# Kernel tuning notes

Hardware: AMD Instinct MI355X
Metric: run time of the kernel (lower is better)

Reference implementation:

```python
import jax, jax.numpy as jnp
import numpy as np

N = 50000      # nodes
E = 800000     # edges
D = 128        # node_dim
H = 4          # heads
C = 64         # hidden_dim per head
B = 64         # graphs in batch
OUT = 10       # output_dim
SLOPE = 0.2    # GATConv leaky_relu negative slope (PyG default)


def gat_conv(x, src, dst, W, a_src, a_dst, bias, concat):
    """One PyG-style GATConv layer. src/dst already include self-loops."""
    n = x.shape[0]
    h = (x @ W).reshape(n, H, C)                       # [N,H,C]
    al_s = jnp.sum(h * a_src, axis=-1)                  # [N,H]
    al_d = jnp.sum(h * a_dst, axis=-1)                  # [N,H]
    e = jax.nn.leaky_relu(al_s[src] + al_d[dst], SLOPE)  # [E+N,H]
    m = jax.ops.segment_max(e, dst, num_segments=n)      # per-target-node max
    e = jnp.exp(e - m[dst])
    den = jax.ops.segment_sum(e, dst, num_segments=n)
    alpha = e / (den[dst] + 1e-16)                       # [E+N,H]
    msg = h[src] * alpha[:, :, None]                     # [E+N,H,C]
    out = jax.ops.segment_sum(msg, dst, num_segments=n)  # [N,H,C]
    out = out.reshape(n, H * C) if concat else out.mean(axis=1)
    return out + bias


def gat_forward(x, edge_index, batch, W0, b0, as0, ad0, W1, b1, as1, ad1,
                W2, b2, as2, ad2, pW1, pb1, pW2, pb2):
    n = x.shape[0]
    loop = jnp.arange(n, dtype=edge_index.dtype)
    src = jnp.concatenate([edge_index[0], loop])
    dst = jnp.concatenate([edge_index[1], loop])

    h = gat_conv(x, src, dst, W0, as0, ad0, b0, concat=True)
    h = jax.nn.elu(h)                                    # dropout = identity (eval)
    h = gat_conv(h, src, dst, W1, as1, ad1, b1, concat=True)
    h = jax.nn.elu(h)
    h = gat_conv(h, src, dst, W2, as2, ad2, b2, concat=False)  # [N,C]

    # global_mean_pool
    sums = jax.ops.segment_sum(h, batch, num_segments=B)        # [B,C]
    cnt = jax.ops.segment_sum(jnp.ones((n,), h.dtype), batch, num_segments=B)
    pooled = sums / jnp.maximum(cnt, 1.0)[:, None]

    # predictor MLP
    z = jax.nn.relu(pooled @ pW1 + pb1)
    return z @ pW2 + pb2                                        # [B,OUT]


def setup_inputs() -> dict:
    key = jax.random.key(0)
    ks = jax.random.split(key, 24)
    gl = lambda k, shp, fan: (jax.random.normal(k, shp, jnp.float32) / np.float32(np.sqrt(fan)))
    x = jax.random.normal(ks[0], (N, D), jnp.float32)
    edge_index = jax.random.randint(ks[1], (2, E), 0, N, dtype=jnp.int32)
    batch = jnp.sort(jax.random.randint(ks[2], (N,), 0, B, dtype=jnp.int32))
    return dict(
        x=x, edge_index=edge_index, batch=batch,
        W0=gl(ks[3], (D, H * C), D), b0=jnp.zeros((H * C,), jnp.float32),
        as0=gl(ks[4], (H, C), C), ad0=gl(ks[5], (H, C), C),
        W1=gl(ks[6], (H * C, H * C), H * C), b1=jnp.zeros((H * C,), jnp.float32),
        as1=gl(ks[7], (H, C), C), ad1=gl(ks[8], (H, C), C),
        W2=gl(ks[9], (H * C, H * C), H * C), b2=jnp.zeros((C,), jnp.float32),
        as2=gl(ks[10], (H, C), C), ad2=gl(ks[11], (H, C), C),
        pW1=gl(ks[12], (C, C // 2), C), pb1=jnp.zeros((C // 2,), jnp.float32),
        pW2=gl(ks[13], (C // 2, OUT), C // 2), pb2=jnp.zeros((OUT,), jnp.float32),
    )


def reference(x, edge_index, batch, W0, b0, as0, ad0, W1, b1, as1, ad1,
              W2, b2, as2, ad2, pW1, pb1, pW2, pb2):
    return gat_forward(x, edge_index, batch, W0, b0, as0, ad0, W1, b1, as1, ad1,
                       W2, b2, as2, ad2, pW1, pb1, pW2, pb2)
```

## Files before the change

kernel.cpp:

```cpp
#include <hip/hip_runtime.h>
#include <hip/hip_fp16.h>
#include <cstdint>

#define N_NODES 50000
#define E_EDGES 800000
#define HC 256
#define B_GR 64
#define OUT_DIM 10
#define SLOPE 0.2f
#define NBLK_SCAN ((N_NODES + 255) / 256)

using f16x8 = __attribute__((ext_vector_type(8))) _Float16;
using f32x4 = __attribute__((ext_vector_type(4))) float;

#define GLOAD_LDS16(gsrc, ldst) \
    __builtin_amdgcn_global_load_lds((const __attribute__((address_space(1))) void*)(gsrc), \
        (__attribute__((address_space(3))) void*)(ldst), 16, 0, 0)

__device__ inline void wsplit_one(const float* W, _Float16* wh, _Float16* wl,
                                  int K, int i) {
    int k = i >> 8, n = i & 255;
    float v = W[i];
    _Float16 h = (_Float16)v;
    _Float16 l = (_Float16)(v - (float)h);
    int oidx = ((((k >> 5) * 256 + n) * 4) + ((k >> 3) & 3)) * 8 + (k & 7);
    wh[oidx] = h;
    wl[oidx] = l;
}

__global__ void prep_split(const float* __restrict__ x,
        _Float16* __restrict__ xhi, _Float16* __restrict__ xlo,
        const float* __restrict__ W0, _Float16* __restrict__ w0h, _Float16* __restrict__ w0l,
        const float* __restrict__ W1, _Float16* __restrict__ w1h, _Float16* __restrict__ w1l,
        const float* __restrict__ W2, _Float16* __restrict__ w2h, _Float16* __restrict__ w2l) {
    const int NX = N_NODES * 128;
    int i = blockIdx.x * 256 + threadIdx.x;
    if (i < NX) {
        float v = x[i];
        _Float16 h = (_Float16)v;
        xhi[i] = h;
        xlo[i] = (_Float16)(v - (float)h);
        return;
    }
    int j = i - NX;
    if (j < 128 * 256) { wsplit_one(W0, w0h, w0l, 128, j); return; }
    j -= 128 * 256;
    if (j < 256 * 256) { wsplit_one(W1, w1h, w1l, 256, j); return; }
    j -= 256 * 256;
    if (j < 256 * 256) { wsplit_one(W2, w2h, w2l, 256, j); return; }
}

template<int K, int TERMS>
__global__ __launch_bounds__(256) void gemm16(const _Float16* __restrict__ Ahi,
        const _Float16* __restrict__ Alo,
        const _Float16* __restrict__ wt_hi, const _Float16* __restrict__ wt_lo,
        __half* __restrict__ h_half,
        const float* __restrict__ a_src, const float* __restrict__ a_dst,
        float* __restrict__ al_s, float* __restrict__ al_d, int M) {
    __shared__ _Float16 abuf[2][2][64][64];
    int tid = threadIdx.x;
    int w = tid >> 6;
    int l = tid & 63;
    int rr = l & 15;
    int kg = l >> 4;
    int row0 = blockIdx.x * 64;
    int srow = tid >> 3;
    int sgs  = tid & 7;

    f32x4 acc[4][4] = {};
    const int NT = K / 64;

    auto stage = [&](int buf, int t) {
        int k0 = t * 64;
#pragma unroll
        for (int i = 0; i < 2; ++i) {
            int row = i * 32 + srow;
            int g = sgs ^ (row & 7);
            int gr = min(row0 + row, M - 1);
            char* dst = (char*)abuf + buf * 16384 + i * 4096 + w * 1024;
            GLOAD_LDS16(&Ahi[(size_t)gr * K + k0 + g * 8], dst);
            if constexpr (TERMS == 3)
                GLOAD_LDS16(&Alo[(size_t)gr * K + k0 + g * 8], dst + 8192);
        }
    };

    stage(0, 0);
    __syncthreads();
    int cur = 0;
    for (int t = 0; t < NT; ++t) {
        if (t + 1 < NT) stage(cur ^ 1, t + 1);
        const _Float16* base_hi = &abuf[cur][0][0][0];
        const _Float16* base_lo = &abuf[cur][1][0][0];
#pragma unroll
        for (int c = 0; c < 2; ++c) {
            f16x8 ah[4], alo_[4];
#pragma unroll
            for (int fm = 0; fm < 4; ++fm) {
                int row = fm * 16 + rr;
                int gsw = ((c * 4 + kg) ^ (row & 7));
                ah[fm] = *(const f16x8*)&base_hi[row * 64 + gsw * 8];
                if constexpr (TERMS == 3)
                    alo_[fm] = *(const f16x8*)&base_lo[row * 64 + gsw * 8];
            }
            int chunk = t * 2 + c;
#pragma unroll
            for (int fn = 0; fn < 4; ++fn) {
                int col = w * 64 + fn * 16 + rr;
                size_t boff = (((size_t)chunk * 256 + col) * 4 + kg) * 8;
                f16x8 bh = *(const f16x8*)&wt_hi[boff];
                f16x8 bl = *(const f16x8*)&wt_lo[boff];
#pragma unroll
                for (int fm = 0; fm < 4; ++fm) {
                    acc[fm][fn] = __builtin_amdgcn_mfma_f32_16x16x32_f16(ah[fm], bh, acc[fm][fn], 0, 0, 0);
                    acc[fm][fn] = __builtin_amdgcn_mfma_f32_16x16x32_f16(ah[fm], bl, acc[fm][fn], 0, 0, 0);
                    if constexpr (TERMS == 3)
                        acc[fm][fn] = __builtin_amdgcn_mfma_f32_16x16x32_f16(alo_[fm], bh, acc[fm][fn], 0, 0, 0);
                }
            }
        }
        __syncthreads();
        cur ^= 1;
    }

    int head = w;
    float asv[4], adv[4];
#pragma unroll
    for (int fn = 0; fn < 4; ++fn) {
        asv[fn] = a_src[head * 64 + fn * 16 + rr];
        adv[fn] = a_dst[head * 64 + fn * 16 + rr];
    }
#pragma unroll
    for (int fm = 0; fm < 4; ++fm) {
#pragma unroll
        for (int r = 0; r < 4; ++r) {
            int row = fm * 16 + kg * 4 + r;
            int gr = row0 + row;
            float ps = acc[fm][0][r] * asv[0] + acc[fm][1][r] * asv[1]
                     + acc[fm][2][r] * asv[2] + acc[fm][3][r] * asv[3];
            float pd = acc[fm][0][r] * adv[0] + acc[fm][1][r] * adv[1]
                     + acc[fm][2][r] * adv[2] + acc[fm][3][r] * adv[3];
#pragma unroll
            for (int off = 1; off < 16; off <<= 1) {
                ps += __shfl_xor(ps, off, 64);
                pd += __shfl_xor(pd, off, 64);
            }
            if (gr < M) {
#pragma unroll
                for (int fn = 0; fn < 4; ++fn)
                    h_half[(size_t)gr * HC + w * 64 + fn * 16 + rr] = __float2half(acc[fm][fn][r]);
                if (rr == 0) {
                    al_s[gr * 4 + head] = ps;
                    al_d[gr * 4 + head] = pd;
                }
            }
        }
    }
}

__global__ void init_cnt(int* cnt) {
    int i = blockIdx.x * blockDim.x + threadIdx.x;
    if (i < N_NODES) cnt[i] = 1;
}
__global__ void hist_kernel(const int* __restrict__ dsts, int* cnt) {
    int i = blockIdx.x * blockDim.x + threadIdx.x;
    if (i < E_EDGES) atomicAdd(&cnt[dsts[i]], 1);
}
__global__ __launch_bounds__(256) void scan_bsum(const int* __restrict__ cnt,
                                                 int* __restrict__ bsum) {
    __shared__ int ws[4];
    int t = threadIdx.x;
    int i = blockIdx.x * 256 + t;
    int v = (i < N_NODES) ? cnt[i] : 0;
#pragma unroll
    for (int off = 1; off < 64; off <<= 1) v += __shfl_xor(v, off, 64);
    if ((t & 63) == 0) ws[t >> 6] = v;
    __syncthreads();
    if (t == 0) bsum[blockIdx.x] = ws[0] + ws[1] + ws[2] + ws[3];
}
__global__ __launch_bounds__(256) void scan_boff(const int* __restrict__ bsum,
                                                 int* __restrict__ boff) {
    __shared__ int s[256];
    int t = threadIdx.x;
    int v = (t < NBLK_SCAN) ? bsum[t] : 0;
    s[t] = v;
    __syncthreads();
    for (int off = 1; off < 256; off <<= 1) {
        int u = (t >= off) ? s[t - off] : 0;
        __syncthreads();
        s[t] += u;
        __syncthreads();
    }
    if (t < NBLK_SCAN) boff[t] = s[t] - v;
}
__global__ __launch_bounds__(256) void scan_final(const int* __restrict__ cnt,
        const int* __restrict__ boff, int* __restrict__ row_ptr,
        int* __restrict__ cursor) {
    __shared__ int s[256];
    int b = blockIdx.x, t = threadIdx.x;
    int i = b * 256 + t;
    int v = (i < N_NODES) ? cnt[i] : 0;
    s[t] = v;
    __syncthreads();
    for (int off = 1; off < 256; off <<= 1) {
        int u = (t >= off) ? s[t - off] : 0;
        __syncthreads();
        s[t] += u;
        __syncthreads();
    }
    int rp = boff[b] + s[t] - v;
    if (i < N_NODES) { row_ptr[i] = rp; cursor[i] = rp; }
    if (i == N_NODES - 1) row_ptr[N_NODES] = rp + v;
}
__global__ void scatter_kernel(const int* __restrict__ srcs, const int* __restrict__ dsts,
                               int* cursor, int* col) {
    int i = blockIdx.x * blockDim.x + threadIdx.x;
    if (i >= E_EDGES + N_NODES) return;
    int s, d;
    if (i < E_EDGES) { s = srcs[i]; d = dsts[i]; }
    else             { s = d = i - E_EDGES; }
    int pos = atomicAdd(&cursor[d], 1);
    col[pos] = s;
}

__global__ __launch_bounds__(256) void agg_kernel(const __half* __restrict__ hh,
        const float* __restrict__ al_s, const float* __restrict__ al_d,
        const int* __restrict__ row_ptr, const int* __restrict__ col,
        const float* __restrict__ bias, _Float16* __restrict__ out_h,
        float* __restrict__ out_f, int mode) {
    __shared__ int   lds_col[4][64];
    __shared__ float lds_alpha[4][64][4];
    int wid  = threadIdx.x >> 6;
    int lane = threadIdx.x & 63;
    int hf   = lane >> 5;
    int ln   = lane & 31;
    int nodeA = blockIdx.x * 8 + wid * 2;
    int nodeB = nodeA + 1;
    int sA = row_ptr[nodeA], eA = row_ptr[nodeA + 1];
    int sB = row_ptr[nodeB], eB = row_ptr[nodeB + 1];
    int degA = eA - sA, degB = eB - sB;

    if (degA <= 32 && degB <= 32) {
        int node  = hf ? nodeB : nodeA;
        int start = hf ? sB : sA;
        int deg   = hf ? degB : degA;
        int degmax = max(degA, degB);
        const float4 ald = *(const float4*)&al_d[node * 4];
        bool active = ln < deg;
        int s = active ? col[start + ln] : 0;
        float4 as = *(const float4*)&al_s[s * 4];
        float e0 = as.x + ald.x; e0 = e0 > 0.f ? e0 : SLOPE * e0;
        float e1 = as.y + ald.y; e1 = e1 > 0.f ? e1 : SLOPE * e1;
        float e2 = as.z + ald.z; e2 = e2 > 0.f ? e2 : SLOPE * e2;
        float e3 = as.w + ald.w; e3 = e3 > 0.f ? e3 : SLOPE * e3;
        float m0 = active ? e0 : -1e30f, m1 = active ? e1 : -1e30f;
        float m2 = active ? e2 : -1e30f, m3 = active ? e3 : -1e30f;
#pragma unroll
        for (int off = 1; off < 32; off <<= 1) {
            m0 = fmaxf(m0, __shfl_xor(m0, off, 64));
            m1 = fmaxf(m1, __shfl_xor(m1, off, 64));
            m2 = fmaxf(m2, __shfl_xor(m2, off, 64));
            m3 = fmaxf(m3, __shfl_xor(m3, off, 64));
        }
        float x0 = active ? expf(e0 - m0) : 0.f;
        float x1 = active ? expf(e1 - m1) : 0.f;
        float x2 = active ? expf(e2 - m2) : 0.f;
        float x3 = active ? expf(e3 - m3) : 0.f;
        float d0 = x0, d1 = x1, d2 = x2, d3 = x3;
#pragma unroll
        for (int off = 1; off < 32; off <<= 1) {
            d0 += __shfl_xor(d0, off, 64);
            d1 += __shfl_xor(d1, off, 64);
            d2 += __shfl_xor(d2, off, 64);
            d3 += __shfl_xor(d3, off, 64);
        }
        float4 a4;
        a4.x = x0 / (d0 + 1e-16f); a4.y = x1 / (d1 + 1e-16f);
        a4.z = x2 / (d2 + 1e-16f); a4.w = x3 / (d3 + 1e-16f);
        int e = hf * 32 + ln;
        lds_col[wid][e] = s;
        *(float4*)&lds_alpha[wid][e][0] = a4;
        int head = ln >> 3;
        int ch0 = ln * 8;
        float acc[8] = {0.f, 0.f, 0.f, 0.f, 0.f, 0.f, 0.f, 0.f};
        int ebase = hf * 32;
        for (int t0 = 0; t0 < degmax; t0 += 4) {
            float wv[4]; float4 raw[4];
#pragma unroll
            for (int k = 0; k < 4; ++k) {
                int t = t0 + k;
                int tt = min(t, deg - 1);
                int s2 = lds_col[wid][ebase + tt];
                wv[k] = (t < deg) ? lds_alpha[wid][ebase + tt][head] : 0.f;
                raw[k] = *(const float4*)&hh[(size_t)s2 * HC + ch0];
            }
#pragma unroll
            for (int k = 0; k < 4; ++k) {
                const __half2* hp = (const __half2*)&raw[k];
                float2 f0 = __half22float2(hp[0]);
                float2 f1 = __half22float2(hp[1]);
                float2 f2 = __half22float2(hp[2]);
                float2 f3 = __half22float2(hp[3]);
                acc[0] = fmaf(wv[k], f0.x, acc[0]); acc[1] = fmaf(wv[k], f0.y, acc[1]);
                acc[2] = fmaf(wv[k], f1.x, acc[2]); acc[3] = fmaf(wv[k], f1.y, acc[3]);
                acc[4] = fmaf(wv[k], f2.x, acc[4]); acc[5] = fmaf(wv[k], f2.y, acc[5]);
                acc[6] = fmaf(wv[k], f3.x, acc[6]); acc[7] = fmaf(wv[k], f3.y, acc[7]);
            }
        }
        if (mode == 0) {
            float b8[8];
            *(float4*)&b8[0] = *(const float4*)&bias[ch0];
            *(float4*)&b8[4] = *(const float4*)&bias[ch0 + 4];
            _Float16 v[8];
#pragma unroll
            for (int j = 0; j < 8; ++j) {
                float t = acc[j] + b8[j];
                v[j] = (_Float16)(t > 0.f ? t : expm1f(t));
            }
            *(float4*)&out_h[(size_t)node * HC + ch0] = *(float4*)v;
        } else {
#pragma unroll
            for (int j = 0; j < 8; ++j) {
                acc[j] += __shfl_xor(acc[j], 8, 64);
                acc[j] += __shfl_xor(acc[j], 16, 64);
            }
            if (ln < 8) {
                float v[8];
#pragma unroll
                for (int j = 0; j < 8; ++j)
                    v[j] = acc[j] * 0.25f + bias[ln * 8 + j];
                *(float4*)&out_f[(size_t)node * 64 + ln * 8]     = *(float4*)&v[0];
                *(float4*)&out_f[(size_t)node * 64 + ln * 8 + 4] = *(float4*)&v[4];
            }
        }
        return;
    }

    for (int nn = 0; nn < 2; ++nn) {
        int node = nodeA + nn;
        int start = row_ptr[node], end = row_ptr[node + 1];
        int deg = end - start;
        const float4 ald = *(const float4*)&al_d[node * 4];
        int head = lane >> 4;
        float ald_h = head == 0 ? ald.x : head == 1 ? ald.y : head == 2 ? ald.z : ald.w;
        float ax = 0.f, ay = 0.f, az = 0.f, aw = 0.f;

        if (deg <= 64) {
            int j = start + lane;
            bool active = j < end;
            int s = active ? col[j] : 0;
            float4 as = *(const float4*)&al_s[s * 4];
            float e0 = as.x + ald.x; e0 = e0 > 0.f ? e0 : SLOPE * e0;
            float e1 = as.y + ald.y; e1 = e1 > 0.f ? e1 : SLOPE * e1;
            float e2 = as.z + ald.z; e2 = e2 > 0.f ? e2 : SLOPE * e2;
            float e3 = as.w + ald.w; e3 = e3 > 0.f ? e3 : SLOPE * e3;
            float m0 = active ? e0 : -1e30f, m1 = active ? e1 : -1e30f;
            float m2 = active ? e2 : -1e30f, m3 = active ? e3 : -1e30f;
#pragma unroll
            for (int off = 1; off < 64; off <<= 1) {
                m0 = fmaxf(m0, __shfl_xor(m0, off, 64));
                m1 = fmaxf(m1, __shfl_xor(m1, off, 64));
                m2 = fmaxf(m2, __shfl_xor(m2, off, 64));
                m3 = fmaxf(m3, __shfl_xor(m3, off, 64));
            }
            float x0 = active ? expf(e0 - m0) : 0.f;
            float x1 = active ? expf(e1 - m1) : 0.f;
            float x2 = active ? expf(e2 - m2) : 0.f;
            float x3 = active ? expf(e3 - m3) : 0.f;
            float d0 = x0, d1 = x1, d2 = x2, d3 = x3;
#pragma unroll
            for (int off = 1; off < 64; off <<= 1) {
                d0 += __shfl_xor(d0, off, 64);
                d1 += __shfl_xor(d1, off, 64);
                d2 += __shfl_xor(d2, off, 64);
                d3 += __shfl_xor(d3, off, 64);
            }
            float4 a4;
            a4.x = x0 / (d0 + 1e-16f); a4.y = x1 / (d1 + 1e-16f);
            a4.z = x2 / (d2 + 1e-16f); a4.w = x3 / (d3 + 1e-16f);
            lds_col[wid][lane] = s;
            *(float4*)&lds_alpha[wid][lane][0] = a4;
            for (int t0 = 0; t0 < deg; t0 += 8) {
                int nr = deg - t0;
                float wv[8]; float2 raw[8];
#pragma unroll
                for (int k = 0; k < 8; ++k) {
                    if (k < nr) {
                        int s2 = lds_col[wid][t0 + k];
                        wv[k] = lds_alpha[wid][t0 + k][head];
                        raw[k] = *(const float2*)&hh[(size_t)s2 * HC + lane * 4];
                    } else {
                        wv[k] = 0.f;
                        raw[k] = make_float2(0.f, 0.f);
                    }
                }
#pragma unroll
                for (int k = 0; k < 8; ++k) {
                    float2 f0 = __half22float2(*(__half2*)&raw[k].x);
                    float2 f1 = __half22float2(*(__half2*)&raw[k].y);
                    ax = fmaf(wv[k], f0.x, ax); ay = fmaf(wv[k], f0.y, ay);
                    az = fmaf(wv[k], f1.x, az); aw = fmaf(wv[k], f1.y, aw);
                }
            }
        } else {
            float m0 = -1e30f, m1 = -1e30f, m2 = -1e30f, m3 = -1e30f;
            for (int j = start + lane; j < end; j += 64) {
                int s = col[j];
                float4 as = *(const float4*)&al_s[s * 4];
                float e0 = as.x + ald.x; e0 = e0 > 0.f ? e0 : SLOPE * e0;
                float e1 = as.y + ald.y; e1 = e1 > 0.f ? e1 : SLOPE * e1;
                float e2 = as.z + ald.z; e2 = e2 > 0.f ? e2 : SLOPE * e2;
                float e3 = as.w + ald.w; e3 = e3 > 0.f ? e3 : SLOPE * e3;
                m0 = fmaxf(m0, e0); m1 = fmaxf(m1, e1);
                m2 = fmaxf(m2, e2); m3 = fmaxf(m3, e3);
            }
#pragma unroll
            for (int off = 1; off < 64; off <<= 1) {
                m0 = fmaxf(m0, __shfl_xor(m0, off, 64));
                m1 = fmaxf(m1, __shfl_xor(m1, off, 64));
                m2 = fmaxf(m2, __shfl_xor(m2, off, 64));
                m3 = fmaxf(m3, __shfl_xor(m3, off, 64));
            }
            float d0 = 0.f, d1 = 0.f, d2 = 0.f, d3 = 0.f;
            for (int j = start + lane; j < end; j += 64) {
                int s = col[j];
                float4 as = *(const float4*)&al_s[s * 4];
                float e0 = as.x + ald.x; e0 = e0 > 0.f ? e0 : SLOPE * e0;
                float e1 = as.y + ald.y; e1 = e1 > 0.f ? e1 : SLOPE * e1;
                float e2 = as.z + ald.z; e2 = e2 > 0.f ? e2 : SLOPE * e2;
                float e3 = as.w + ald.w; e3 = e3 > 0.f ? e3 : SLOPE * e3;
                d0 += expf(e0 - m0); d1 += expf(e1 - m1);
                d2 += expf(e2 - m2); d3 += expf(e3 - m3);
            }
#pragma unroll
            for (int off = 1; off < 64; off <<= 1) {
                d0 += __shfl_xor(d0, off, 64);
                d1 += __shfl_xor(d1, off, 64);
                d2 += __shfl_xor(d2, off, 64);
                d3 += __shfl_xor(d3, off, 64);
            }
            float inv0 = 1.f / (d0 + 1e-16f), inv1 = 1.f / (d1 + 1e-16f);
            float inv2 = 1.f / (d2 + 1e-16f), inv3 = 1.f / (d3 + 1e-16f);
            float m_h   = head == 0 ? m0   : head == 1 ? m1   : head == 2 ? m2   : m3;
            float inv_h = head == 0 ? inv0 : head == 1 ? inv1 : head == 2 ? inv2 : inv3;
            for (int jb = start; jb < end; jb += 64) {
                int j = jb + lane;
                int cs = (j < end) ? col[j] : 0;
                int cnt2 = min(64, end - jb);
                for (int t = 0; t < cnt2; ++t) {
                    int s = __shfl(cs, t, 64);
                    float als2 = al_s[s * 4 + head];
                    float e = als2 + ald_h; e = e > 0.f ? e : SLOPE * e;
                    float wv = expf(e - m_h) * inv_h;
                    float2 raw = *(const float2*)&hh[(size_t)s * HC + lane * 4];
                    float2 f0 = __half22float2(*(__half2*)&raw.x);
                    float2 f1 = __half22float2(*(__half2*)&raw.y);
                    ax = fmaf(wv, f0.x, ax); ay = fmaf(wv, f0.y, ay);
                    az = fmaf(wv, f1.x, az); aw = fmaf(wv, f1.y, aw);
                }
            }
        }

        if (mode == 0) {
            float4 b4 = *(const float4*)&bias[lane * 4];
            float vx = ax + b4.x; vx = vx > 0.f ? vx : expm1f(vx);
            float vy = ay + b4.y; vy = vy > 0.f ? vy : expm1f(vy);
            float vz = az + b4.z; vz = vz > 0.f ? vz : expm1f(vz);
            float vw = aw + b4.w; vw = vw > 0.f ? vw : expm1f(vw);
            _Float16 v[4] = {(_Float16)vx, (_Float16)vy, (_Float16)vz, (_Float16)vw};
            *(float2*)&out_h[(size_t)node * HC + lane * 4] = *(float2*)v;
        } else {
#pragma unroll
            for (int off = 16; off < 64; off <<= 1) {
                ax += __shfl_xor(ax, off, 64);
                ay += __shfl_xor(ay, off, 64);
                az += __shfl_xor(az, off, 64);
                aw += __shfl_xor(aw, off, 64);
            }
            if (lane < 16) {
                float4 b4 = *(const float4*)&bias[lane * 4];
                float4 v = make_float4(ax * 0.25f + b4.x, ay * 0.25f + b4.y,
                                       az * 0.25f + b4.z, aw * 0.25f + b4.w);
                *(float4*)&out_f[(size_t)node * 64 + lane * 4] = v;
            }
        }
    }
}

__global__ __launch_bounds__(1024) void pool_kernel(const float* __restrict__ act,
        const int* __restrict__ batch, float* __restrict__ pooled) {
    __shared__ float part[16][64];
    int b = blockIdx.x;
    int warp = threadIdx.x >> 6;
    int lane = threadIdx.x & 63;
    int lo = 0, hi = N_NODES;
    while (lo < hi) { int mid = (lo + hi) >> 1; if (batch[mid] < b) lo = mid + 1; else hi = mid; }
    int s = lo;
    lo = 0; hi = N_NODES;
    while (lo < hi) { int mid = (lo + hi) >> 1; if (batch[mid] < b + 1) lo = mid + 1; else hi = mid; }
    int e = lo;
    float sum = 0.f;
    for (int n = s + warp; n < e; n += 16)
        sum += act[(size_t)n * 64 + lane];
    part[warp][lane] = sum;
    __syncthreads();
    if (threadIdx.x < 64) {
        float t = 0.f;
#pragma unroll
        for (int r = 0; r < 16; ++r) t += part[r][lane];
        pooled[b * 64 + lane] = t;
    }
}

__global__ __launch_bounds__(64) void mlp_kernel(const float* __restrict__ pooled,
        const int* __restrict__ batch,
        const float* __restrict__ pW1, const float* __restrict__ pb1,
        const float* __restrict__ pW2, const float* __restrict__ pb2,
        float* __restrict__ outp) {
    __shared__ float p[64];
    __shared__ float z[32];
    int b = blockIdx.x, t = threadIdx.x;
    int lo = 0, hi = N_NODES;
    while (lo < hi) { int mid = (lo + hi) >> 1; if (batch[mid] < b) lo = mid + 1; else hi = mid; }
    int s = lo;
    lo = 0; hi = N_NODES;
    while (lo < hi) { int mid = (lo + hi) >> 1; if (batch[mid] < b + 1) lo = mid + 1; else hi = mid; }
    int e = lo;
    float inv = 1.f / (float)max(e - s, 1);
    p[t] = pooled[b * 64 + t] * inv;
    __syncthreads();
    if (t < 32) {
        float s2 = pb1[t];
        for (int c = 0; c < 64; ++c) s2 += p[c] * pW1[c * 32 + t];
        z[t] = s2 > 0.f ? s2 : 0.f;
    }
    __syncthreads();
    if (t < OUT_DIM) {
        float s2 = pb2[t];
        for (int k = 0; k < 32; ++k) s2 += z[k] * pW2[k * 10 + t];
        outp[b * 10 + t] = s2;
    }
}

extern "C" void kernel_launch(void* const* d_in, const int* in_sizes, int n_in,
                              void* d_out, int out_size, void* d_ws, size_t ws_size,
                              hipStream_t stream) {
    const float* x    = (const float*)d_in[0];
    const int*   ei   = (const int*)d_in[1];
    const int*   batch= (const int*)d_in[2];
    const float* W0   = (const float*)d_in[3];
    const float* b0   = (const float*)d_in[4];
    const float* as0  = (const float*)d_in[5];
    const float* ad0  = (const float*)d_in[6];
    const float* W1   = (const float*)d_in[7];
    const float* b1   = (const float*)d_in[8];
    const float* as1  = (const float*)d_in[9];
    const float* ad1  = (const float*)d_in[10];
    const float* W2   = (const float*)d_in[11];
    const float* b2   = (const float*)d_in[12];
    const float* as2  = (const float*)d_in[13];
    const float* ad2  = (const float*)d_in[14];
    const float* pW1  = (const float*)d_in[15];
    const float* pb1  = (const float*)d_in[16];
    const float* pW2  = (const float*)d_in[17];
    const float* pb2  = (const float*)d_in[18];
    float* out = (float*)d_out;

    char* ws = (char*)d_ws;
    size_t off = 0;
    auto alloc = [&](size_t bytes) -> void* {
        void* p = ws + off;
        off += (bytes + 255) & ~(size_t)255;
        return p;
    };
    __half*    h_half = (__half*)alloc((size_t)N_NODES * HC * 2);
    _Float16*  act_h  = (_Float16*)alloc((size_t)N_NODES * HC * 2);
    float*     act_f  = (float*)alloc((size_t)N_NODES * 64 * 4);
    _Float16*  xhi    = (_Float16*)alloc((size_t)N_NODES * 128 * 2);
    _Float16*  xlo    = (_Float16*)alloc((size_t)N_NODES * 128 * 2);
    float* als    = (float*)alloc((size_t)N_NODES * 4 * 4);
    float* ald    = (float*)alloc((size_t)N_NODES * 4 * 4);
    int*   cnt    = (int*)alloc((size_t)N_NODES * 4);
    int*   row_ptr= (int*)alloc((size_t)(N_NODES + 1) * 4);
    int*   cursor = (int*)alloc((size_t)N_NODES * 4);
    int*   col    = (int*)alloc((size_t)(E_EDGES + N_NODES) * 4);
    float* pooled = (float*)alloc((size_t)B_GR * 64 * 4);
    int*   bsum   = (int*)alloc((size_t)NBLK_SCAN * 4);
    int*   boff   = (int*)alloc((size_t)NBLK_SCAN * 4);
    _Float16* w0h = (_Float16*)alloc((size_t)128 * 256 * 2);
    _Float16* w0l = (_Float16*)alloc((size_t)128 * 256 * 2);
    _Float16* w1h = (_Float16*)alloc((size_t)256 * 256 * 2);
    _Float16* w1l = (_Float16*)alloc((size_t)256 * 256 * 2);
    _Float16* w2h = (_Float16*)alloc((size_t)256 * 256 * 2);
    _Float16* w2l = (_Float16*)alloc((size_t)256 * 256 * 2);

    const int* srcs = ei;
    const int* dsts = ei + E_EDGES;

    const int PREP_N = N_NODES * 128 + 128 * 256 + 256 * 256 + 256 * 256;
    prep_split<<<(PREP_N + 255) / 256, 256, 0, stream>>>(
        x, xhi, xlo, W0, w0h, w0l, W1, w1h, w1l, W2, w2h, w2l);

    init_cnt<<<(N_NODES + 255) / 256, 256, 0, stream>>>(cnt);
    hist_kernel<<<(E_EDGES + 255) / 256, 256, 0, stream>>>(dsts, cnt);
    scan_bsum<<<NBLK_SCAN, 256, 0, stream>>>(cnt, bsum);
    scan_boff<<<1, 256, 0, stream>>>(bsum, boff);
    scan_final<<<NBLK_SCAN, 256, 0, stream>>>(cnt, boff, row_ptr, cursor);
    scatter_kernel<<<(E_EDGES + N_NODES + 255) / 256, 256, 0, stream>>>(srcs, dsts, cursor, col);

    int gblk = (N_NODES + 63) / 64;
    int nblk = (N_NODES + 7) / 8;

    gemm16<128, 3><<<gblk, 256, 0, stream>>>(xhi, xlo, w0h, w0l, h_half, as0, ad0, als, ald, N_NODES);
    agg_kernel<<<nblk, 256, 0, stream>>>(h_half, als, ald, row_ptr, col, b0, act_h, act_f, 0);
    gemm16<256, 2><<<gblk, 256, 0, stream>>>(act_h, nullptr, w1h, w1l, h_half, as1, ad1, als, ald, N_NODES);
    agg_kernel<<<nblk, 256, 0, stream>>>(h_half, als, ald, row_ptr, col, b1, act_h, act_f, 0);
    gemm16<256, 2><<<gblk, 256, 0, stream>>>(act_h, nullptr, w2h, w2l, h_half, as2, ad2, als, ald, N_NODES);
    agg_kernel<<<nblk, 256, 0, stream>>>(h_half, als, ald, row_ptr, col, b2, act_h, act_f, 1);

    pool_kernel<<<B_GR, 1024, 0, stream>>>(act_f, batch, pooled);
    mlp_kernel<<<B_GR, 64, 0, stream>>>(pooled, batch, pW1, pb1, pW2, pb2, out);
}
```

Before: 423.1 us.

## Fuse GAT aggregation with next layer GEMM and merge pool/MLP kernels

Layers 1 and 2 now aggregate 64 destination nodes per block straight into a swizzled LDS activation tile, apply bias and ELU, and run the next layer's MFMA GEMM and attention projections from that tile. This removes the global write and re-read of the fp16 activation buffer and two kernel launches. Ping-pong h/al buffers avoid read-write hazards. The cnt init is folded into prep_split and pool and MLP are merged into one kernel. The trade-off is heavy LDS use (32KB+) and a long serial aggregation phase per block before the GEMM, with fewer blocks than before, which may reduce occupancy and latency hiding in the gather.

```diff
diff --git a/kernel.cpp b/kernel.cpp
--- a/kernel.cpp
+++ b/kernel.cpp
@@ -32,7 +32,8 @@
         _Float16* __restrict__ xhi, _Float16* __restrict__ xlo,
         const float* __restrict__ W0, _Float16* __restrict__ w0h, _Float16* __restrict__ w0l,
         const float* __restrict__ W1, _Float16* __restrict__ w1h, _Float16* __restrict__ w1l,
-        const float* __restrict__ W2, _Float16* __restrict__ w2h, _Float16* __restrict__ w2l) {
+        const float* __restrict__ W2, _Float16* __restrict__ w2h, _Float16* __restrict__ w2l,
+        int* __restrict__ cnt) {
     const int NX = N_NODES * 128;
     int i = blockIdx.x * 256 + threadIdx.x;
     if (i < NX) {
@@ -48,6 +49,8 @@
     if (j < 256 * 256) { wsplit_one(W1, w1h, w1l, 256, j); return; }
     j -= 256 * 256;
     if (j < 256 * 256) { wsplit_one(W2, w2h, w2l, 256, j); return; }
+    j -= 256 * 256;
+    if (j < N_NODES) cnt[j] = 1;
 }
 
 template<int K, int TERMS>
@@ -157,10 +160,326 @@
     }
 }
 
-__global__ void init_cnt(int* cnt) {
-    int i = blockIdx.x * blockDim.x + threadIdx.x;
-    if (i < N_NODES) cnt[i] = 1;
-}
+__global__ __launch_bounds__(256) void fused_agg_gemm(
+        const __half* __restrict__ hh,
+        const float* __restrict__ al_s, const float* __restrict__ al_d,
+        const int* __restrict__ row_ptr, const int* __restrict__ col,
+        const float* __restrict__ bias,
+        const _Float16* __restrict__ wt_hi, const _Float16* __restrict__ wt_lo,
+        __half* __restrict__ h_out,
+        const float* __restrict__ a_srcn, const float* __restrict__ a_dstn,
+        float* __restrict__ al_s_out, float* __restrict__ al_d_out, int M) {
+    __shared__ _Float16 a_act[64][256];
+    __shared__ int   lds_col[4][64];
+    __shared__ float lds_alpha[4][64][4];
+    int tid = threadIdx.x;
+    int wid = tid >> 6;
+    int lane = tid & 63;
+    int hf = lane >> 5;
+    int ln = lane & 31;
+    int row0 = blockIdx.x * 64;
+
+    for (int it = 0; it < 8; ++it) {
+        int nodeA = row0 + it * 8 + wid * 2;
+        int nodeB = nodeA + 1;
+        int rA = it * 8 + wid * 2, rB = rA + 1;
+        bool vA = nodeA < M, vB = nodeB < M;
+        int sA = 0, eA = 0, sB = 0, eB = 0;
+        if (vA) { sA = row_ptr[nodeA]; eA = row_ptr[nodeA + 1]; }
+        if (vB) { sB = row_ptr[nodeB]; eB = row_ptr[nodeB + 1]; }
+        int degA = eA - sA, degB = eB - sB;
+
+        if (degA <= 32 && degB <= 32) {
+            int node  = hf ? nodeB : nodeA;
+            int r     = hf ? rB : rA;
+            int start = hf ? sB : sA;
+            int deg   = hf ? degB : degA;
+            bool valid = hf ? vB : vA;
+            int degmax = max(degA, degB);
+            float4 ald = valid ? *(const float4*)&al_d[node * 4]
+                               : make_float4(0.f, 0.f, 0.f, 0.f);
+            bool active = ln < deg;
+            int s = active ? col[start + ln] : 0;
+            float4 as = *(const float4*)&al_s[s * 4];
+            float e0 = as.x + ald.x; e0 = e0 > 0.f ? e0 : SLOPE * e0;
+            float e1 = as.y + ald.y; e1 = e1 > 0.f ? e1 : SLOPE * e1;
+            float e2 = as.z + ald.z; e2 = e2 > 0.f ? e2 : SLOPE * e2;
+            float e3 = as.w + ald.w; e3 = e3 > 0.f ? e3 : SLOPE * e3;
+            float m0 = active ? e0 : -1e30f, m1 = active ? e1 : -1e30f;
+            float m2 = active ? e2 : -1e30f, m3 = active ? e3 : -1e30f;
+#pragma unroll
+            for (int off = 1; off < 32; off <<= 1) {
+                m0 = fmaxf(m0, __shfl_xor(m0, off, 64));
+                m1 = fmaxf(m1, __shfl_xor(m1, off, 64));
+                m2 = fmaxf(m2, __shfl_xor(m2, off, 64));
+                m3 = fmaxf(m3, __shfl_xor(m3, off, 64));
+            }
+            float x0 = active ? expf(e0 - m0) : 0.f;
+            float x1 = active ? expf(e1 - m1) : 0.f;
+            float x2 = active ? expf(e2 - m2) : 0.f;
+            float x3 = active ? expf(e3 - m3) : 0.f;
+            float d0 = x0, d1 = x1, d2 = x2, d3 = x3;
+#pragma unroll
+            for (int off = 1; off < 32; off <<= 1) {
+                d0 += __shfl_xor(d0, off, 64);
+                d1 += __shfl_xor(d1, off, 64);
+                d2 += __shfl_xor(d2, off, 64);
+                d3 += __shfl_xor(d3, off, 64);
+            }
+            float4 a4;
+            a4.x = x0 / (d0 + 1e-16f); a4.y = x1 / (d1 + 1e-16f);
+            a4.z = x2 / (d2 + 1e-16f); a4.w = x3 / (d3 + 1e-16f);
+            int e = hf * 32 + ln;
+            lds_col[wid][e] = s;
+            *(float4*)&lds_alpha[wid][e][0] = a4;
+            int head = ln >> 3;
+            int ch0 = ln * 8;
+            float acc[8] = {0.f, 0.f, 0.f, 0.f, 0.f, 0.f, 0.f, 0.f};
+            int ebase = hf * 32;
+            for (int t0 = 0; t0 < degmax; t0 += 4) {
+                float wv[4]; float4 raw[4];
+#pragma unroll
+                for (int k = 0; k < 4; ++k) {
+                    int t = t0 + k;
+                    int tt = max(min(t, deg - 1), 0);
+                    int s2 = lds_col[wid][ebase + tt];
+                    wv[k] = (t < deg) ? lds_alpha[wid][ebase + tt][head] : 0.f;
+                    raw[k] = *(const float4*)&hh[(size_t)s2 * HC + ch0];
+                }
+#pragma unroll
+                for (int k = 0; k < 4; ++k) {
+                    const __half2* hp = (const __half2*)&raw[k];
+                    float2 f0 = __half22float2(hp[0]);
+                    float2 f1 = __half22float2(hp[1]);
+                    float2 f2 = __half22float2(hp[2]);
+                    float2 f3 = __half22float2(hp[3]);
+                    acc[0] = fmaf(wv[k], f0.x, acc[0]); acc[1] = fmaf(wv[k], f0.y, acc[1]);
+                    acc[2] = fmaf(wv[k], f1.x, acc[2]); acc[3] = fmaf(wv[k], f1.y, acc[3]);
+                    acc[4] = fmaf(wv[k], f2.x, acc[4]); acc[5] = fmaf(wv[k], f2.y, acc[5]);
+                    acc[6] = fmaf(wv[k], f3.x, acc[6]); acc[7] = fmaf(wv[k], f3.y, acc[7]);
+                }
+            }
+            float b8[8];
+            *(float4*)&b8[0] = *(const float4*)&bias[ch0];
+            *(float4*)&b8[4] = *(const float4*)&bias[ch0 + 4];
+            f16x8 v;
+#pragma unroll
+            for (int j = 0; j < 8; ++j) {
+                float t = acc[j] + b8[j];
+                t = t > 0.f ? t : expm1f(t);
+                v[j] = valid ? (_Float16)t : (_Float16)0.f;
+            }
+            int gs = ln ^ (r & 7);
+            *(f16x8*)&a_act[r][gs * 8] = v;
+        } else {
+            for (int nn = 0; nn < 2; ++nn) {
+                int node = nodeA + nn;
+                int r = rA + nn;
+                bool valid = node < M;
+                int start = 0, end = 0;
+                if (valid) { start = row_ptr[node]; end = row_ptr[node + 1]; }
+                int deg = end - start;
+                float4 ald = valid ? *(const float4*)&al_d[node * 4]
+                                   : make_float4(0.f, 0.f, 0.f, 0.f);
+                int head = lane >> 4;
+                float ald_h = head == 0 ? ald.x : head == 1 ? ald.y : head == 2 ? ald.z : ald.w;
+                float ax = 0.f, ay = 0.f, az = 0.f, aw = 0.f;
+
+                if (deg <= 64) {
+                    int j = start + lane;
+                    bool active = lane < deg;
+                    int s = active ? col[j] : 0;
+                    float4 as = *(const float4*)&al_s[s * 4];
+                    float e0 = as.x + ald.x; e0 = e0 > 0.f ? e0 : SLOPE * e0;
+                    float e1 = as.y + ald.y; e1 = e1 > 0.f ? e1 : SLOPE * e1;
+                    float e2 = as.z + ald.z; e2 = e2 > 0.f ? e2 : SLOPE * e2;
+                    float e3 = as.w + ald.w; e3 = e3 > 0.f ? e3 : SLOPE * e3;
+                    float m0 = active ? e0 : -1e30f, m1 = active ? e1 : -1e30f;
+                    float m2 = active ? e2 : -1e30f, m3 = active ? e3 : -1e30f;
+#pragma unroll
+                    for (int off = 1; off < 64; off <<= 1) {
+                        m0 = fmaxf(m0, __shfl_xor(m0, off, 64));
+                        m1 = fmaxf(m1, __shfl_xor(m1, off, 64));
+                        m2 = fmaxf(m2, __shfl_xor(m2, off, 64));
+                        m3 = fmaxf(m3, __shfl_xor(m3, off, 64));
+                    }
+                    float x0 = active ? expf(e0 - m0) : 0.f;
+                    float x1 = active ? expf(e1 - m1) : 0.f;
+                    float x2 = active ? expf(e2 - m2) : 0.f;
+                    float x3 = active ? expf(e3 - m3) : 0.f;
+                    float d0 = x0, d1 = x1, d2 = x2, d3 = x3;
+#pragma unroll
+                    for (int off = 1; off < 64; off <<= 1) {
+                        d0 += __shfl_xor(d0, off, 64);
+                        d1 += __shfl_xor(d1, off, 64);
+                        d2 += __shfl_xor(d2, off, 64);
+                        d3 += __shfl_xor(d3, off, 64);
+                    }
+                    float4 a4;
+                    a4.x = x0 / (d0 + 1e-16f); a4.y = x1 / (d1 + 1e-16f);
+                    a4.z = x2 / (d2 + 1e-16f); a4.w = x3 / (d3 + 1e-16f);
+                    lds_col[wid][lane] = s;
+                    *(float4*)&lds_alpha[wid][lane][0] = a4;
+                    for (int t0 = 0; t0 < deg; t0 += 8) {
+                        int nr = deg - t0;
+                        float wv[8]; float2 raw[8];
+#pragma unroll
+                        for (int k = 0; k < 8; ++k) {
+                            if (k < nr) {
+                                int s2 = lds_col[wid][t0 + k];
+                                wv[k] = lds_alpha[wid][t0 + k][head];
+                                raw[k] = *(const float2*)&hh[(size_t)s2 * HC + lane * 4];
+                            } else {
+                                wv[k] = 0.f;
+                                raw[k] = make_float2(0.f, 0.f);
+                            }
+                        }
+#pragma unroll
+                        for (int k = 0; k < 8; ++k) {
+                            float2 f0 = __half22float2(*(__half2*)&raw[k].x);
+                            float2 f1 = __half22float2(*(__half2*)&raw[k].y);
+                            ax = fmaf(wv[k], f0.x, ax); ay = fmaf(wv[k], f0.y, ay);
+                            az = fmaf(wv[k], f1.x, az); aw = fmaf(wv[k], f1.y, aw);
+                        }
+                    }
+                } else {
+                    float m0 = -1e30f, m1 = -1e30f, m2 = -1e30f, m3 = -1e30f;
+                    for (int j = start + lane; j < end; j += 64) {
+                        int s = col[j];
+                        float4 as = *(const float4*)&al_s[s * 4];
+                        float e0 = as.x + ald.x; e0 = e0 > 0.f ? e0 : SLOPE * e0;
+                        float e1 = as.y + ald.y; e1 = e1 > 0.f ? e1 : SLOPE * e1;
+                        float e2 = as.z + ald.z; e2 = e2 > 0.f ? e2 : SLOPE * e2;
+                        float e3 = as.w + ald.w; e3 = e3 > 0.f ? e3 : SLOPE * e3;
+                        m0 = fmaxf(m0, e0); m1 = fmaxf(m1, e1);
+                        m2 = fmaxf(m2, e2); m3 = fmaxf(m3, e3);
+                    }
+#pragma unroll
+                    for (int off = 1; off < 64; off <<= 1) {
+                        m0 = fmaxf(m0, __shfl_xor(m0, off, 64));
+                        m1 = fmaxf(m1, __shfl_xor(m1, off, 64));
+                        m2 = fmaxf(m2, __shfl_xor(m2, off, 64));
+                        m3 = fmaxf(m3, __shfl_xor(m3, off, 64));
+                    }
+                    float d0 = 0.f, d1 = 0.f, d2 = 0.f, d3 = 0.f;
+                    for (int j = start + lane; j < end; j += 64) {
+                        int s = col[j];
+                        float4 as = *(const float4*)&al_s[s * 4];
+                        float e0 = as.x + ald.x; e0 = e0 > 0.f ? e0 : SLOPE * e0;
+                        float e1 = as.y + ald.y; e1 = e1 > 0.f ? e1 : SLOPE * e1;
+                        float e2 = as.z + ald.z; e2 = e2 > 0.f ? e2 : SLOPE * e2;
+                        float e3 = as.w + ald.w; e3 = e3 > 0.f ? e3 : SLOPE * e3;
+                        d0 += expf(e0 - m0); d1 += expf(e1 - m1);
+                        d2 += expf(e2 - m2); d3 += expf(e3 - m3);
+                    }
+#pragma unroll
+                    for (int off = 1; off < 64; off <<= 1) {
+                        d0 += __shfl_xor(d0, off, 64);
+                        d1 += __shfl_xor(d1, off, 64);
+                        d2 += __shfl_xor(d2, off, 64);
+                        d3 += __shfl_xor(d3, off, 64);
+                    }
+                    float inv0 = 1.f / (d0 + 1e-16f), inv1 = 1.f / (d1 + 1e-16f);
+                    float inv2 = 1.f / (d2 + 1e-16f), inv3 = 1.f / (d3 + 1e-16f);
+                    float m_h   = head == 0 ? m0   : head == 1 ? m1   : head == 2 ? m2   : m3;
+                    float inv_h = head == 0 ? inv0 : head == 1 ? inv1 : head == 2 ? inv2 : inv3;
+                    for (int jb = start; jb < end; jb += 64) {
+                        int j = jb + lane;
+                        int cs = (j < end) ? col[j] : 0;
+                        int cnt2 = min(64, end - jb);
+                        for (int t = 0; t < cnt2; ++t) {
+                            int s = __shfl(cs, t, 64);
+                            float als2 = al_s[s * 4 + head];
+                            float e = als2 + ald_h; e = e > 0.f ? e : SLOPE * e;
+                            float wv = expf(e - m_h) * inv_h;
+                            float2 raw = *(const float2*)&hh[(size_t)s * HC + lane * 4];
+                            float2 f0 = __half22float2(*(__half2*)&raw.x);
+                            float2 f1 = __half22float2(*(__half2*)&raw.y);
+                            ax = fmaf(wv, f0.x, ax); ay = fmaf(wv, f0.y, ay);
+                            az = fmaf(wv, f1.x, az); aw = fmaf(wv, f1.y, aw);
+                        }
+                    }
+                }
+                float4 b4 = *(const float4*)&bias[lane * 4];
+                float vx = ax + b4.x; vx = vx > 0.f ? vx : expm1f(vx);
+                float vy = ay + b4.y; vy = vy > 0.f ? vy : expm1f(vy);
+                float vz = az + b4.z; vz = vz > 0.f ? vz : expm1f(vz);
+                float vw = aw + b4.w; vw = vw > 0.f ? vw : expm1f(vw);
+                _Float16 v[4];
+                v[0] = valid ? (_Float16)vx : (_Float16)0.f;
+                v[1] = valid ? (_Float16)vy : (_Float16)0.f;
+                v[2] = valid ? (_Float16)vz : (_Float16)0.f;
+                v[3] = valid ? (_Float16)vw : (_Float16)0.f;
+                int grp = lane >> 1, half = lane & 1;
+                int gs = grp ^ (r & 7);
+                *(float2*)&a_act[r][gs * 8 + half * 4] = *(float2*)v;
+            }
+        }
+    }
+    __syncthreads();
+
+    int w = wid;
+    int rr = lane & 15;
+    int kg = lane >> 4;
+    f32x4 acc[4][4] = {};
+#pragma unroll
+    for (int ch = 0; ch < 8; ++ch) {
+        f16x8 ah[4];
+#pragma unroll
+        for (int fm = 0; fm < 4; ++fm) {
+            int row = fm * 16 + rr;
+            int gsw = ((ch * 4 + kg) ^ (row & 7));
+            ah[fm] = *(const f16x8*)&a_act[row][gsw * 8];
+        }
+#pragma unroll
+        for (int fn = 0; fn < 4; ++fn) {
+            int c2 = w * 64 + fn * 16 + rr;
+            size_t boff = (((size_t)ch * 256 + c2) * 4 + kg) * 8;
+            f16x8 bh = *(const f16x8*)&wt_hi[boff];
+            f16x8 bl = *(const f16x8*)&wt_lo[boff];
+#pragma unroll
+            for (int fm = 0; fm < 4; ++fm) {
+                acc[fm][fn] = __builtin_amdgcn_mfma_f32_16x16x32_f16(ah[fm], bh, acc[fm][fn], 0, 0, 0);
+                acc[fm][fn] = __builtin_amdgcn_mfma_f32_16x16x32_f16(ah[fm], bl, acc[fm][fn], 0, 0, 0);
+            }
+        }
+    }
+
+    int head = w;
+    float asv[4], adv[4];
+#pragma unroll
+    for (int fn = 0; fn < 4; ++fn) {
+        asv[fn] = a_srcn[head * 64 + fn * 16 + rr];
+        adv[fn] = a_dstn[head * 64 + fn * 16 + rr];
+    }
+#pragma unroll
+    for (int fm = 0; fm < 4; ++fm) {
+#pragma unroll
+        for (int r = 0; r < 4; ++r) {
+            int row = fm * 16 + kg * 4 + r;
+            int gr = row0 + row;
+            float ps = acc[fm][0][r] * asv[0] + acc[fm][1][r] * asv[1]
+                     + acc[fm][2][r] * asv[2] + acc[fm][3][r] * asv[3];
+            float pd = acc[fm][0][r] * adv[0] + acc[fm][1][r] * adv[1]
+                     + acc[fm][2][r] * adv[2] + acc[fm][3][r] * adv[3];
+#pragma unroll
+            for (int off = 1; off < 16; off <<= 1) {
+                ps += __shfl_xor(ps, off, 64);
+                pd += __shfl_xor(pd, off, 64);
+            }
+            if (gr < M) {
+#pragma unroll
+                for (int fn = 0; fn < 4; ++fn)
+                    h_out[(size_t)gr * HC + w * 64 + fn * 16 + rr] = __float2half(acc[fm][fn][r]);
+                if (rr == 0) {
+                    al_s_out[gr * 4 + head] = ps;
+                    al_d_out[gr * 4 + head] = pd;
+                }
+            }
+        }
+    }
+}
+
 __global__ void hist_kernel(const int* __restrict__ dsts, int* cnt) {
     int i = blockIdx.x * blockDim.x + threadIdx.x;
     if (i < E_EDGES) atomicAdd(&cnt[dsts[i]], 1);
@@ -222,11 +541,10 @@
     col[pos] = s;
 }
 
-__global__ __launch_bounds__(256) void agg_kernel(const __half* __restrict__ hh,
+__global__ __launch_bounds__(256) void agg_final(const __half* __restrict__ hh,
         const float* __restrict__ al_s, const float* __restrict__ al_d,
         const int* __restrict__ row_ptr, const int* __restrict__ col,
-        const float* __restrict__ bias, _Float16* __restrict__ out_h,
-        float* __restrict__ out_f, int mode) {
+        const float* __restrict__ bias, float* __restrict__ out_f) {
     __shared__ int   lds_col[4][64];
     __shared__ float lds_alpha[4][64][4];
     int wid  = threadIdx.x >> 6;
@@ -288,7 +606,7 @@
 #pragma unroll
             for (int k = 0; k < 4; ++k) {
                 int t = t0 + k;
-                int tt = min(t, deg - 1);
+                int tt = max(min(t, deg - 1), 0);
                 int s2 = lds_col[wid][ebase + tt];
                 wv[k] = (t < deg) ? lds_alpha[wid][ebase + tt][head] : 0.f;
                 raw[k] = *(const float4*)&hh[(size_t)s2 * HC + ch0];
@@ -306,31 +624,18 @@
                 acc[6] = fmaf(wv[k], f3.x, acc[6]); acc[7] = fmaf(wv[k], f3.y, acc[7]);
             }
         }
-        if (mode == 0) {
-            float b8[8];
-            *(float4*)&b8[0] = *(const float4*)&bias[ch0];
-            *(float4*)&b8[4] = *(const float4*)&bias[ch0 + 4];
-            _Float16 v[8];
-#pragma unroll
-            for (int j = 0; j < 8; ++j) {
-                float t = acc[j] + b8[j];
-                v[j] = (_Float16)(t > 0.f ? t : expm1f(t));
-            }
-            *(float4*)&out_h[(size_t)node * HC + ch0] = *(float4*)v;
-        } else {
-#pragma unroll
-            for (int j = 0; j < 8; ++j) {
-                acc[j] += __shfl_xor(acc[j], 8, 64);
-                acc[j] += __shfl_xor(acc[j], 16, 64);
-            }
-            if (ln < 8) {
-                float v[8];
-#pragma unroll
-                for (int j = 0; j < 8; ++j)
-                    v[j] = acc[j] * 0.25f + bias[ln * 8 + j];
-                *(float4*)&out_f[(size_t)node * 64 + ln * 8]     = *(float4*)&v[0];
-                *(float4*)&out_f[(size_t)node * 64 + ln * 8 + 4] = *(float4*)&v[4];
-            }
+#pragma unroll
+        for (int j = 0; j < 8; ++j) {
+            acc[j] += __shfl_xor(acc[j], 8, 64);
+            acc[j] += __shfl_xor(acc[j], 16, 64);
+        }
+        if (ln < 8) {
+            float v[8];
+#pragma unroll
+            for (int j = 0; j < 8; ++j)
+                v[j] = acc[j] * 0.25f + bias[ln * 8 + j];
+            *(float4*)&out_f[(size_t)node * 64 + ln * 8]     = *(float4*)&v[0];
+            *(float4*)&out_f[(size_t)node * 64 + ln * 8 + 4] = *(float4*)&v[4];
         }
         return;
     }
@@ -343,7 +648,6 @@
         int head = lane >> 4;
         float ald_h = head == 0 ? ald.x : head == 1 ? ald.y : head == 2 ? ald.z : ald.w;
         float ax = 0.f, ay = 0.f, az = 0.f, aw = 0.f;
-
         if (deg <= 64) {
             int j = start + lane;
             bool active = j < end;
@@ -459,36 +763,30 @@
                 }
             }
         }
-
-        if (mode == 0) {
+#pragma unroll
+        for (int off = 16; off < 64; off <<= 1) {
+            ax += __shfl_xor(ax, off, 64);
+            ay += __shfl_xor(ay, off, 64);
+            az += __shfl_xor(az, off, 64);
+            aw += __shfl_xor(aw, off, 64);
+        }
+        if (lane < 16) {
             float4 b4 = *(const float4*)&bias[lane * 4];
-            float vx = ax + b4.x; vx = vx > 0.f ? vx : expm1f(vx);
-            float vy = ay + b4.y; vy = vy > 0.f ? vy : expm1f(vy);
-            float vz = az + b4.z; vz = vz > 0.f ? vz : expm1f(vz);
-            float vw = aw + b4.w; vw = vw > 0.f ? vw : expm1f(vw);
-            _Float16 v[4] = {(_Float16)vx, (_Float16)vy, (_Float16)vz, (_Float16)vw};
-            *(float2*)&out_h[(size_t)node * HC + lane * 4] = *(float2*)v;
-        } else {
-#pragma unroll
-            for (int off = 16; off < 64; off <<= 1) {
-                ax += __shfl_xor(ax, off, 64);
-                ay += __shfl_xor(ay, off, 64);
-                az += __shfl_xor(az, off, 64);
-                aw += __shfl_xor(aw, off, 64);
-            }
-            if (lane < 16) {
-                float4 b4 = *(const float4*)&bias[lane * 4];
-                float4 v = make_float4(ax * 0.25f + b4.x, ay * 0.25f + b4.y,
-                                       az * 0.25f + b4.z, aw * 0.25f + b4.w);
-                *(float4*)&out_f[(size_t)node * 64 + lane * 4] = v;
-            }
-        }
-    }
-}
-
-__global__ __launch_bounds__(1024) void pool_kernel(const float* __restrict__ act,
-        const int* __restrict__ batch, float* __restrict__ pooled) {
+            float4 v = make_float4(ax * 0.25f + b4.x, ay * 0.25f + b4.y,
+                                   az * 0.25f + b4.z, aw * 0.25f + b4.w);
+            *(float4*)&out_f[(size_t)node * 64 + lane * 4] = v;
+        }
+    }
+}
+
+__global__ __launch_bounds__(1024) void poolmlp_kernel(const float* __restrict__ act,
+        const int* __restrict__ batch,
+        const float* __restrict__ pW1, const float* __restrict__ pb1,
+        const float* __restrict__ pW2, const float* __restrict__ pb2,
+        float* __restrict__ outp) {
     __shared__ float part[16][64];
+    __shared__ float p[64];
+    __shared__ float z[32];
     int b = blockIdx.x;
     int warp = threadIdx.x >> 6;
     int lane = threadIdx.x & 63;
@@ -503,30 +801,13 @@
         sum += act[(size_t)n * 64 + lane];
     part[warp][lane] = sum;
     __syncthreads();
-    if (threadIdx.x < 64) {
-        float t = 0.f;
-#pragma unroll
-        for (int r = 0; r < 16; ++r) t += part[r][lane];
-        pooled[b * 64 + lane] = t;
-    }
-}
-
-__global__ __launch_bounds__(64) void mlp_kernel(const float* __restrict__ pooled,
-        const int* __restrict__ batch,
-        const float* __restrict__ pW1, const float* __restrict__ pb1,
-        const float* __restrict__ pW2, const float* __restrict__ pb2,
-        float* __restrict__ outp) {
-    __shared__ float p[64];
-    __shared__ float z[32];
-    int b = blockIdx.x, t = threadIdx.x;
-    int lo = 0, hi = N_NODES;
-    while (lo < hi) { int mid = (lo + hi) >> 1; if (batch[mid] < b) lo = mid + 1; else hi = mid; }
-    int s = lo;
-    lo = 0; hi = N_NODES;
-    while (lo < hi) { int mid = (lo + hi) >> 1; if (batch[mid] < b + 1) lo = mid + 1; else hi = mid; }
-    int e = lo;
-    float inv = 1.f / (float)max(e - s, 1);
-    p[t] = pooled[b * 64 + t] * inv;
+    int t = threadIdx.x;
+    if (t < 64) {
+        float tt = 0.f;
+#pragma unroll
+        for (int r = 0; r < 16; ++r) tt += part[r][t];
+        p[t] = tt / (float)max(e - s, 1);
+    }
     __syncthreads();
     if (t < 32) {
         float s2 = pb1[t];
@@ -572,18 +853,19 @@
         off += (bytes + 255) & ~(size_t)255;
         return p;
     };
-    __half*    h_half = (__half*)alloc((size_t)N_NODES * HC * 2);
-    _Float16*  act_h  = (_Float16*)alloc((size_t)N_NODES * HC * 2);
+    __half*    h_a    = (__half*)alloc((size_t)N_NODES * HC * 2);
+    __half*    h_b    = (__half*)alloc((size_t)N_NODES * HC * 2);
     float*     act_f  = (float*)alloc((size_t)N_NODES * 64 * 4);
     _Float16*  xhi    = (_Float16*)alloc((size_t)N_NODES * 128 * 2);
     _Float16*  xlo    = (_Float16*)alloc((size_t)N_NODES * 128 * 2);
-    float* als    = (float*)alloc((size_t)N_NODES * 4 * 4);
-    float* ald    = (float*)alloc((size_t)N_NODES * 4 * 4);
+    float* als_a  = (float*)alloc((size_t)N_NODES * 4 * 4);
+    float* ald_a  = (float*)alloc((size_t)N_NODES * 4 * 4);
+    float* als_b  = (float*)alloc((size_t)N_NODES * 4 * 4);
+    float* ald_b  = (float*)alloc((size_t)N_NODES * 4 * 4);
     int*   cnt    = (int*)alloc((size_t)N_NODES * 4);
     int*   row_ptr= (int*)alloc((size_t)(N_NODES + 1) * 4);
     int*   cursor = (int*)alloc((size_t)N_NODES * 4);
     int*   col    = (int*)alloc((size_t)(E_EDGES + N_NODES) * 4);
-    float* pooled = (float*)alloc((size_t)B_GR * 64 * 4);
     int*   bsum   = (int*)alloc((size_t)NBLK_SCAN * 4);
     int*   boff   = (int*)alloc((size_t)NBLK_SCAN * 4);
     _Float16* w0h = (_Float16*)alloc((size_t)128 * 256 * 2);
@@ -596,11 +878,10 @@
     const int* srcs = ei;
     const int* dsts = ei + E_EDGES;
 
-    const int PREP_N = N_NODES * 128 + 128 * 256 + 256 * 256 + 256 * 256;
+    const int PREP_N = N_NODES * 128 + 128 * 256 + 256 * 256 + 256 * 256 + N_NODES;
     prep_split<<<(PREP_N + 255) / 256, 256, 0, stream>>>(
-        x, xhi, xlo, W0, w0h, w0l, W1, w1h, w1l, W2, w2h, w2l);
-
-    init_cnt<<<(N_NODES + 255) / 256, 256, 0, stream>>>(cnt);
+        x, xhi, xlo, W0, w0h, w0l, W1, w1h, w1l, W2, w2h, w2l, cnt);
+
     hist_kernel<<<(E_EDGES + 255) / 256, 256, 0, stream>>>(dsts, cnt);
     scan_bsum<<<NBLK_SCAN, 256, 0, stream>>>(cnt, bsum);
     scan_boff<<<1, 256, 0, stream>>>(bsum, boff);
@@ -610,13 +891,12 @@
     int gblk = (N_NODES + 63) / 64;
     int nblk = (N_NODES + 7) / 8;
 
-    gemm16<128, 3><<<gblk, 256, 0, stream>>>(xhi, xlo, w0h, w0l, h_half, as0, ad0, als, ald, N_NODES);
-    agg_kernel<<<nblk, 256, 0, stream>>>(h_half, als, ald, row_ptr, col, b0, act_h, act_f, 0);
-    gemm16<256, 2><<<gblk, 256, 0, stream>>>(act_h, nullptr, w1h, w1l, h_half, as1, ad1, als, ald, N_NODES);
-    agg_kernel<<<nblk, 256, 0, stream>>>(h_half, als, ald, row_ptr, col, b1, act_h, act_f, 0);
-    gemm16<256, 2><<<gblk, 256, 0, stream>>>(act_h, nullptr, w2h, w2l, h_half, as2, ad2, als, ald, N_NODES);
-    agg_kernel<<<nblk, 256, 0, stream>>>(h_half, als, ald, row_ptr, col, b2, act_h, act_f, 1);
-
-    pool_kernel<<<B_GR, 1024, 0, stream>>>(act_f, batch, pooled);
-    mlp_kernel<<<B_GR, 64, 0, stream>>>(pooled, batch, pW1, pb1, pW2, pb2, out);
-}
+    gemm16<128, 3><<<gblk, 256, 0, stream>>>(xhi, xlo, w0h, w0l, h_a, as0, ad0, als_a, ald_a, N_NODES);
+    fused_agg_gemm<<<gblk, 256, 0, stream>>>(h_a, als_a, ald_a, row_ptr, col, b0,
+                                             w1h, w1l, h_b, as1, ad1, als_b, ald_b, N_NODES);
+    fused_agg_gemm<<<gblk, 256, 0, stream>>>(h_b, als_b, ald_b, row_ptr, col, b1,
+                                             w2h, w2l, h_a, as2, ad2, als_a, ald_a, N_NODES);
+    agg_final<<<nblk, 256, 0, stream>>>(h_a, als_a, ald_a, row_ptr, col, b2, act_f);
+
+    poolmlp_kernel<<<B_GR, 1024, 0, stream>>>(act_f, batch, pW1, pb1, pW2, pb2, out);
+}
```

Measured after the change: 477.1 us. 1.13x slower.
